# Kernel tuning notes

Hardware: AMD Instinct MI355X
Metric: run time of the kernel (lower is better)

Reference implementation:

```python
import jax, jax.numpy as jnp
import numpy as np
import math

B, D, A = 16384, 1024, 512   # batch, input_dim, n_atoms
N_ITER = 16
K_MIN = 0.01
EPS = 1e-06


def _soft(z, th):
    # sign(z) * relu(|z| - th)
    return jnp.sign(z) * jax.nn.relu(jnp.abs(z) - th)


def setup_inputs() -> dict:
    key = jax.random.key(0)
    ks = jax.random.split(key, 16)
    def lin(k, fan_in, fan_out):
        lim = 1.0 / math.sqrt(fan_in)
        kw, kb = jax.random.split(k)
        W = jax.random.uniform(kw, (fan_in, fan_out), jnp.float32, -lim, lim)
        b = jax.random.uniform(kb, (fan_out,), jnp.float32, -lim, lim)
        return W, b
    x = jax.random.normal(ks[0], (B, D), jnp.float32)
    W_proj, b_proj = lin(ks[1], D, A)
    W_rec, _ = lin(ks[2], A, A)  # bias=False
    log_threshold = jnp.full((A,), math.log(0.1), jnp.float32)
    W_pres, _ = lin(ks[3], A, 2 * A)
    b_pres = jnp.zeros((2 * A,), jnp.float32)  # presence_head_bias_init=0
    W_sign, _ = lin(ks[4], A, A)
    b_sign = jnp.zeros((A,), jnp.float32)      # sign_head_bias_init=0
    W_g1, b_g1 = lin(ks[5], D + 1 + A, A)
    W_g2, b_g2 = lin(ks[6], A, A)
    W_k, b_k = lin(ks[7], A, A)
    W_t, b_t = lin(ks[8], A, A)
    return dict(x=x, W_proj=W_proj, b_proj=b_proj, W_rec=W_rec,
                log_threshold=log_threshold, W_pres=W_pres, b_pres=b_pres,
                W_sign=W_sign, b_sign=b_sign, W_g1=W_g1, b_g1=b_g1,
                W_g2=W_g2, b_g2=b_g2, W_k=W_k, b_k=b_k, W_t=W_t, b_t=b_t)


def reference(x, W_proj, b_proj, W_rec, log_threshold, W_pres, b_pres,
              W_sign, b_sign, W_g1, b_g1, W_g2, b_g2, W_k, b_k, W_t, b_t):
    x_flat = x.reshape(x.shape[0], -1)                      # [B, D]
    input_scale = jnp.linalg.norm(x_flat, axis=1, keepdims=True)  # [B, 1]
    x_shape = x_flat / (input_scale + EPS)

    drive = x_shape @ W_proj + b_proj                       # [B, A]
    threshold = jnp.exp(log_threshold)[None, :]             # [1, A]
    h0 = _soft(drive, threshold)

    def step(h, _):
        proposal = drive + h @ W_rec
        return _soft(proposal, threshold), None
    h_delta, _ = jax.lax.scan(step, h0, None, length=N_ITER - 1)

    shape_ctx = jax.lax.stop_gradient(h_delta)              # shape_detach_to_gamma=True
    gain_scalar = jnp.log(input_scale + EPS)                # gain_feature='log_l2'
    gamma_in = jnp.concatenate([x_flat, gain_scalar, shape_ctx], axis=1)  # [B, D+1+A]
    h_gamma = jax.nn.relu(gamma_in @ W_g1 + b_g1)
    h_gamma = jax.nn.relu(h_gamma @ W_g2 + b_g2)

    k_out = jax.nn.softplus(h_gamma @ W_k + b_k) + K_MIN    # k_max=inf -> no clamp
    theta_out = jax.nn.softplus(h_gamma @ W_t + b_t) + 1e-4

    presence_logits = (h_delta @ W_pres + b_pres).reshape(x.shape[0], A, 2)[:, :, None, :]  # [B, A, 1, 2]
    sign_scores = (h_delta @ W_sign + b_sign)[:, :, None]   # [B, A, 1]

    return (k_out[:, :, None], theta_out[:, :, None], presence_logits, sign_scores,
            input_scale[:, 0], h_delta, h_gamma)
```

## Files before the change

### kernel.cpp

```cpp
#include <hip/hip_runtime.h>
#include <hip/hip_fp8.h>

typedef __attribute__((ext_vector_type(8))) short short8;
typedef __attribute__((ext_vector_type(4))) float f32x4;

#define NB 16384
#define DDIM 1024
#define AD 512

static __device__ __forceinline__ unsigned short f2bf(float f){
  unsigned int u = __float_as_uint(f);
  u += 0x7FFFu + ((u >> 16) & 1u);
  return (unsigned short)(u >> 16);
}
static __device__ __forceinline__ float bf2f(short s){
  return __uint_as_float(((unsigned int)(unsigned short)s) << 16);
}
static __device__ __forceinline__ unsigned long long pack4(float a, float b, float c, float d){
  return (unsigned long long)f2bf(a) | ((unsigned long long)f2bf(b) << 16)
       | ((unsigned long long)f2bf(c) << 32) | ((unsigned long long)f2bf(d) << 48);
}
static __device__ __forceinline__ unsigned char f2e4(float f){
  return __hip_fp8_e4m3(f).__x;
}
static __device__ __forceinline__ unsigned int pack4f8(float a, float b, float c, float d){
  return (unsigned)f2e4(a) | ((unsigned)f2e4(b) << 8) | ((unsigned)f2e4(c) << 16) | ((unsigned)f2e4(d) << 24);
}
static __device__ __forceinline__ float softplusf(float z){
  return fmaxf(z, 0.f) + log1pf(expf(-fabsf(z)));
}
static __device__ __forceinline__ float softf(float z, float th){
  return copysignf(fmaxf(fabsf(z) - th, 0.f), z);
}

static __device__ __forceinline__ void bar_lds(){
  __builtin_amdgcn_sched_barrier(0);
  asm volatile("s_waitcnt lgkmcnt(0)" ::: "memory");
  __builtin_amdgcn_s_barrier();
  __builtin_amdgcn_sched_barrier(0);
}

__global__ void pack_all(const float* __restrict__ W_proj, const float* __restrict__ W_rec,
                         const float* __restrict__ W_pres, const float* __restrict__ W_sign,
                         const float* __restrict__ W_g1,   const float* __restrict__ W_g2,
                         const float* __restrict__ W_k,    const float* __restrict__ W_t,
                         unsigned char* __restrict__ ws){
  int t = blockIdx.x * 256 + threadIdx.x;
  const float* W; size_t off; int KS, NT, ldn, isbf; float scl = 16.f;
  if      (t < 32768) {              W = W_rec;                   off = 0;       KS = 16; NT = 32; ldn = 512;  isbf = 1; }
  else if (t < 98304) { t -= 32768;  W = W_proj;                  off = 524288;  KS = 32; NT = 32; ldn = 512;  isbf = 0; }
  else if (t < 163840){ t -= 98304;  W = W_pres;                  off = 1048576; KS = 16; NT = 64; ldn = 1024; isbf = 0; }
  else if (t < 196608){ t -= 163840; W = W_sign;                  off = 1572864; KS = 16; NT = 32; ldn = 512;  isbf = 0; }
  else if (t < 262144){ t -= 196608; W = W_g1;                    off = 1835008; KS = 32; NT = 32; ldn = 512;  isbf = 0; scl = 4.f; }
  else if (t < 294912){ t -= 262144; W = W_g1 + (size_t)1025*512; off = 2359296; KS = 16; NT = 32; ldn = 512;  isbf = 0; }
  else if (t < 327680){ t -= 294912; W = W_g2;                    off = 2621440; KS = 16; NT = 32; ldn = 512;  isbf = 0; }
  else if (t < 360448){ t -= 327680; W = W_k;                     off = 2883584; KS = 16; NT = 32; ldn = 512;  isbf = 0; }
  else if (t < 393216){ t -= 360448; W = W_t;                     off = 3145728; KS = 16; NT = 32; ldn = 512;  isbf = 0; }
  else return;
  int lane = t & 63;
  int frag = t >> 6;
  int ks = frag % KS;
  int nt = frag / KS;
  int col = nt * 16 + (lane & 15);
  int k0 = ks * 32 + ((lane >> 4) << 3);
  const float* src = W + (size_t)k0 * ldn + col;
  if (isbf){
    short8 v;
#pragma unroll
    for (int j = 0; j < 8; ++j) v[j] = (short)f2bf(src[(size_t)j * ldn]);
    *(short8*)(ws + off + ((size_t)frag * 64 + lane) * 16) = v;
  } else {
    unsigned long long v = 0;
#pragma unroll
    for (int j = 0; j < 8; ++j)
      v |= (unsigned long long)f2e4(src[(size_t)j * ldn] * scl) << (8 * j);
    *(unsigned long long*)(ws + off + ((size_t)frag * 64 + lane) * 8) = v;
  }
}

__device__ __forceinline__ void gemm_bf16(const unsigned char* __restrict__ hb,
    const unsigned char* __restrict__ A, int lane, f32x4 acc[2][4]){
  const int c16 = lane & 15;
  const int g16 = (lane >> 4) << 4;
  const int swz = ((c16 & 7) << 4) ^ g16;
  const unsigned char* bp[4];
#pragma unroll
  for (int rf = 0; rf < 4; ++rf) bp[rf] = hb + (size_t)(rf * 16 + c16) * 1024;
  const unsigned char* a0 = A + lane * 16;
  const unsigned char* a1 = A + 16 * 1024 + lane * 16;
  short8 af0 = *(const short8*)a0;
  short8 af1 = *(const short8*)a1;
#pragma unroll
  for (int ks = 0; ks < 16; ++ks){
    short8 c0 = af0, c1 = af1;
    if (ks < 15){
      a0 += 1024; a1 += 1024;
      af0 = *(const short8*)a0;
      af1 = *(const short8*)a1;
    }
    int kb = ks * 64;
    short8 b[4];
#pragma unroll
    for (int rf = 0; rf < 4; ++rf) b[rf] = *(const short8*)(bp[rf] + (kb ^ swz));
    __builtin_amdgcn_s_setprio(1);
#pragma unroll
    for (int rf = 0; rf < 4; ++rf){
      acc[0][rf] = __builtin_amdgcn_mfma_f32_16x16x32_bf16(c0, b[rf], acc[0][rf], 0, 0, 0);
      acc[1][rf] = __builtin_amdgcn_mfma_f32_16x16x32_bf16(c1, b[rf], acc[1][rf], 0, 0, 0);
    }
    __builtin_amdgcn_s_setprio(0);
  }
}

template<int KSRUN, int RS>
__device__ __forceinline__ void gemm_fp8(const unsigned char* __restrict__ bb,
    const unsigned char* __restrict__ A, int kstot, int lane, f32x4 acc[2][4]){
  const int c16 = lane & 15;
  const int g8 = (lane >> 4) << 3;
  const int swz = (c16 << 3) ^ g8;
  const unsigned char* bp[4];
#pragma unroll
  for (int rf = 0; rf < 4; ++rf) bp[rf] = bb + (size_t)(rf * 16 + c16) * RS;
  const unsigned char* a0 = A + lane * 8;
  const unsigned char* a1 = A + (size_t)kstot * 512 + lane * 8;
  long f0 = *(const long*)a0;
  long f1 = *(const long*)a1;
#pragma unroll
  for (int ks = 0; ks < KSRUN; ++ks){
    long c0 = f0, c1 = f1;
    if (ks < KSRUN - 1){
      a0 += 512; a1 += 512;
      f0 = *(const long*)a0;
      f1 = *(const long*)a1;
    }
    int kb = ks * 32;
    long b[4];
#pragma unroll
    for (int rf = 0; rf < 4; ++rf) b[rf] = *(const long*)(bp[rf] + (kb ^ swz));
    __builtin_amdgcn_s_setprio(1);
#pragma unroll
    for (int rf = 0; rf < 4; ++rf){
      acc[0][rf] = __builtin_amdgcn_mfma_f32_16x16x32_fp8_fp8(c0, b[rf], acc[0][rf], 0, 0, 0);
      acc[1][rf] = __builtin_amdgcn_mfma_f32_16x16x32_fp8_fp8(c1, b[rf], acc[1][rf], 0, 0, 0);
    }
    __builtin_amdgcn_s_setprio(0);
  }
}

template<int KSRUN, int RS>
__device__ __forceinline__ void gemm_fp8_dual(const unsigned char* __restrict__ bb,
    const unsigned char* __restrict__ A0, const unsigned char* __restrict__ A1,
    int kstot, int lane, f32x4 acc0[2][4], f32x4 acc1[2][4]){
  const int c16 = lane & 15;
  const int g8 = (lane >> 4) << 3;
  const int swz = (c16 << 3) ^ g8;
  const unsigned char* bp[4];
#pragma unroll
  for (int rf = 0; rf < 4; ++rf) bp[rf] = bb + (size_t)(rf * 16 + c16) * RS;
  const unsigned char* a00 = A0 + lane * 8;
  const unsigned char* a01 = A0 + (size_t)kstot * 512 + lane * 8;
  const unsigned char* a10 = A1 + lane * 8;
  const unsigned char* a11 = A1 + (size_t)kstot * 512 + lane * 8;
  long f00 = *(const long*)a00, f01 = *(const long*)a01;
  long f10 = *(const long*)a10, f11 = *(const long*)a11;
#pragma unroll
  for (int ks = 0; ks < KSRUN; ++ks){
    long c00 = f00, c01 = f01, c10 = f10, c11 = f11;
    if (ks < KSRUN - 1){
      a00 += 512; a01 += 512; a10 += 512; a11 += 512;
      f00 = *(const long*)a00; f01 = *(const long*)a01;
      f10 = *(const long*)a10; f11 = *(const long*)a11;
    }
    int kb = ks * 32;
    long b[4];
#pragma unroll
    for (int rf = 0; rf < 4; ++rf) b[rf] = *(const long*)(bp[rf] + (kb ^ swz));
    __builtin_amdgcn_s_setprio(1);
#pragma unroll
    for (int rf = 0; rf < 4; ++rf){
      acc0[0][rf] = __builtin_amdgcn_mfma_f32_16x16x32_fp8_fp8(c00, b[rf], acc0[0][rf], 0, 0, 0);
      acc0[1][rf] = __builtin_amdgcn_mfma_f32_16x16x32_fp8_fp8(c01, b[rf], acc0[1][rf], 0, 0, 0);
      acc1[0][rf] = __builtin_amdgcn_mfma_f32_16x16x32_fp8_fp8(c10, b[rf], acc1[0][rf], 0, 0, 0);
      acc1[1][rf] = __builtin_amdgcn_mfma_f32_16x16x32_fp8_fp8(c11, b[rf], acc1[1][rf], 0, 0, 0);
    }
    __builtin_amdgcn_s_setprio(0);
  }
}

#define ZERO_ACC(A) { _Pragma("unroll") for (int c_=0;c_<2;++c_) _Pragma("unroll") for(int r_=0;r_<4;++r_){ f32x4 z_ = {0.f,0.f,0.f,0.f}; A[c_][r_]=z_; } }

static __device__ __forceinline__ void tile_write(unsigned char* tile, int row, int colb, f32x4 v){
  *(unsigned long long*)(tile + (size_t)row * 1024 + (colb ^ ((row & 7) << 4))) = pack4(v[0], v[1], v[2], v[3]);
}

static __device__ __forceinline__ void tile_store(const unsigned char* __restrict__ tile,
    float* __restrict__ dst, int ldo, int wid, int lane){
  int row = wid * 4 + (lane >> 4);
  const unsigned char* rp = tile + (size_t)row * 1024;
  float* orow = dst + (size_t)row * ldo;
  int sw = row & 7;
  int l4 = lane & 15;
#pragma unroll
  for (int cb = 0; cb < 4; ++cb){
    short8 v = *(const short8*)(rp + ((size_t)(cb * 16 + (l4 ^ sw))) * 16);
    float* op = orow + (cb * 16 + l4) * 8;
    f32x4 lo, hi;
#pragma unroll
    for (int j = 0; j < 4; ++j){ lo[j] = bf2f(v[j]); hi[j] = bf2f(v[j + 4]); }
    __builtin_nontemporal_store(lo, (f32x4*)op);
    __builtin_nontemporal_store(hi, (f32x4*)(op + 4));
  }
}

__global__ __launch_bounds__(1024, 4) void polar_main(
    const float* __restrict__ x,
    const float* __restrict__ b_proj,
    const float* __restrict__ log_th,
    const float* __restrict__ b_pres,
    const float* __restrict__ b_sign,
    const float* __restrict__ W_g1,
    const float* __restrict__ b_g1,
    const float* __restrict__ b_g2,
    const float* __restrict__ b_k,
    const float* __restrict__ b_t,
    const unsigned char* __restrict__ ws,
    float* __restrict__ out)
{
  __shared__ __align__(128) unsigned char smem[163840];
  unsigned char* hbuf = smem;
  unsigned char* xbuf = smem + 65536;
  unsigned char* aux  = smem + 131072;
  float* recip_s = (float*)aux;
  float* gain_s  = (float*)(aux + 256);

  const unsigned char* Prec  = ws;
  const unsigned char* Pproj = ws + 524288;
  const unsigned char* Ppres = ws + 1048576;
  const unsigned char* Psign = ws + 1572864;
  const unsigned char* Pg1x  = ws + 1835008;
  const unsigned char* Pg1h  = ws + 2359296;
  const unsigned char* Pg2   = ws + 2621440;
  const unsigned char* Pk    = ws + 2883584;
  const unsigned char* Pt    = ws + 3145728;

  const int tid = threadIdx.x;
  const int lane = tid & 63;
  const int wid = tid >> 6;
  const int row0 = blockIdx.x * 64;
  const int c16 = lane & 15;
  const int g2r = (lane >> 4) << 2;

  float* out_k     = out;
  float* out_th    = out + (size_t)NB * AD;
  float* out_pres  = out + (size_t)2 * NB * AD;
  float* out_sign  = out + (size_t)4 * NB * AD;
  float* out_scale = out + (size_t)5 * NB * AD;
  float* out_hd    = out_scale + NB;
  float* out_hg    = out_hd + (size_t)NB * AD;

  {
    int r = tid >> 4, sub = tid & 15;
    const float* xr = x + (size_t)(row0 + r) * DDIM + sub * 64;
    float ss = 0.f;
#pragma unroll
    for (int i = 0; i < 8; ++i){
      f32x4 v0 = __builtin_nontemporal_load((const f32x4*)(xr + i * 8));
      f32x4 v1 = __builtin_nontemporal_load((const f32x4*)(xr + i * 8 + 4));
      ss += v0[0]*v0[0] + v0[1]*v0[1] + v0[2]*v0[2] + v0[3]*v0[3]
          + v1[0]*v1[0] + v1[1]*v1[1] + v1[2]*v1[2] + v1[3]*v1[3];
      unsigned long long w = (unsigned long long)pack4f8(v0[0]*4.f, v0[1]*4.f, v0[2]*4.f, v0[3]*4.f)
                           | ((unsigned long long)pack4f8(v1[0]*4.f, v1[1]*4.f, v1[2]*4.f, v1[3]*4.f) << 32);
      int cbyte = sub * 64 + i * 8;
      *(unsigned long long*)(xbuf + (size_t)r * 1024 + (cbyte ^ ((r & 15) << 3))) = w;
    }
    ss += __shfl_xor(ss, 1);
    ss += __shfl_xor(ss, 2);
    ss += __shfl_xor(ss, 4);
    ss += __shfl_xor(ss, 8);
    if (sub == 0){
      float norm = sqrtf(ss);
      recip_s[r] = 1.f / (norm + 1e-6f);
      gain_s[r]  = logf(norm + 1e-6f);
      __builtin_nontemporal_store(norm, out_scale + row0 + r);
    }
  }
  bar_lds();

  float rn[4], gn[4];
#pragma unroll
  for (int rf = 0; rf < 4; ++rf){
    rn[rf] = recip_s[rf * 16 + c16];
    gn[rf] = gain_s[rf * 16 + c16];
  }

  f32x4 acc[2][4];

  ZERO_ACC(acc);
  gemm_fp8<32, 1024>(xbuf, Pproj + (size_t)(wid * 2) * 32 * 512, 32, lane, acc);

  f32x4 dr[2][4];
  f32x4 th4[2];
#pragma unroll
  for (int cf = 0; cf < 2; ++cf){
    int col0 = wid * 32 + cf * 16 + g2r;
    f32x4 lt = *(const f32x4*)(log_th + col0);
    f32x4 bp = *(const f32x4*)(b_proj + col0);
#pragma unroll
    for (int r = 0; r < 4; ++r) th4[cf][r] = expf(lt[r]);
#pragma unroll
    for (int rf = 0; rf < 4; ++rf)
#pragma unroll
      for (int r = 0; r < 4; ++r)
        dr[cf][rf][r] = acc[cf][rf][r] * (rn[rf] * (1.f / 64.f)) + bp[r];
  }
#pragma unroll
  for (int cf = 0; cf < 2; ++cf){
    int colb = (wid * 32 + cf * 16 + g2r) * 2;
#pragma unroll
    for (int rf = 0; rf < 4; ++rf){
      f32x4 hv;
#pragma unroll
      for (int r = 0; r < 4; ++r) hv[r] = softf(dr[cf][rf][r], th4[cf][r]);
      tile_write(hbuf, rf * 16 + c16, colb, hv);
    }
  }
  bar_lds();

  const unsigned char* Arec = Prec + (size_t)(wid * 2) * 16 * 1024;
#pragma unroll 1
  for (int it = 0; it < 15; ++it){
    ZERO_ACC(acc);
    gemm_bf16(hbuf, Arec, lane, acc);
    bar_lds();
#pragma unroll
    for (int cf = 0; cf < 2; ++cf){
      int col0 = wid * 32 + cf * 16 + g2r;
#pragma unroll
      for (int rf = 0; rf < 4; ++rf){
        int row = rf * 16 + c16;
        f32x4 hv;
#pragma unroll
        for (int r = 0; r < 4; ++r)
          hv[r] = softf(dr[cf][rf][r] + acc[cf][rf][r], th4[cf][r]);
        tile_write(hbuf, row, col0 * 2, hv);
        if (it == 14)
          *(unsigned int*)(aux + (size_t)row * 512 + (col0 ^ (c16 << 3))) =
              pack4f8(hv[0], hv[1], hv[2], hv[3]);
      }
    }
    bar_lds();
  }

  f32x4 acc2[2][4];

  tile_store(hbuf, out_hd + (size_t)row0 * AD, AD, wid, lane);

  ZERO_ACC(acc);
  ZERO_ACC(acc2);
  gemm_fp8_dual<16, 512>(aux,
      Ppres + (size_t)(wid * 2) * 16 * 512,
      Ppres + (size_t)(32 + wid * 2) * 16 * 512, 16, lane, acc, acc2);
  bar_lds();

#pragma unroll
  for (int cf = 0; cf < 2; ++cf){
    int col0 = (wid * 2 + cf) * 16 + g2r;
    f32x4 bv = *(const f32x4*)(b_pres + col0);
    int colb = (wid * 32 + cf * 16 + g2r) * 2;
#pragma unroll
    for (int rf = 0; rf < 4; ++rf){
      f32x4 o;
#pragma unroll
      for (int r = 0; r < 4; ++r) o[r] = acc[cf][rf][r] * (1.f / 16.f) + bv[r];
      tile_write(hbuf, rf * 16 + c16, colb, o);
    }
  }
  bar_lds();
  tile_store(hbuf, out_pres + (size_t)row0 * 1024, 1024, wid, lane);

  ZERO_ACC(acc);
  gemm_fp8<16, 512>(aux, Psign + (size_t)(wid * 2) * 16 * 512, 16, lane, acc);
  bar_lds();

#pragma unroll
  for (int cf = 0; cf < 2; ++cf){
    int col0 = (32 + wid * 2 + cf) * 16 + g2r;
    f32x4 bv = *(const f32x4*)(b_pres + col0);
    int colb = (wid * 32 + cf * 16 + g2r) * 2;
#pragma unroll
    for (int rf = 0; rf < 4; ++rf){
      f32x4 o;
#pragma unroll
      for (int r = 0; r < 4; ++r) o[r] = acc2[cf][rf][r] * (1.f / 16.f) + bv[r];
      tile_write(hbuf, rf * 16 + c16, colb, o);
    }
  }
  bar_lds();
  tile_store(hbuf, out_pres + (size_t)row0 * 1024 + 512, 1024, wid, lane);
  bar_lds();

#pragma unroll
  for (int cf = 0; cf < 2; ++cf){
    int col0 = wid * 32 + cf * 16 + g2r;
    f32x4 bv = *(const f32x4*)(b_sign + col0);
#pragma unroll
    for (int rf = 0; rf < 4; ++rf){
      f32x4 o;
#pragma unroll
      for (int r = 0; r < 4; ++r) o[r] = acc[cf][rf][r] * (1.f / 16.f) + bv[r];
      tile_write(hbuf, rf * 16 + c16, col0 * 2, o);
    }
  }
  bar_lds();
  tile_store(hbuf, out_sign + (size_t)row0 * AD, AD, wid, lane);

  {
    ZERO_ACC(acc);
    gemm_fp8<32, 1024>(xbuf, Pg1x + (size_t)(wid * 2) * 32 * 512, 32, lane, acc);
    gemm_fp8<16, 512>(aux, Pg1h + (size_t)(wid * 2) * 16 * 512, 16, lane, acc);

    f32x4 bv[2], wg[2];
#pragma unroll
    for (int cf = 0; cf < 2; ++cf){
      int col0 = wid * 32 + cf * 16 + g2r;
      bv[cf] = *(const f32x4*)(b_g1 + col0);
      wg[cf] = *(const f32x4*)(W_g1 + (size_t)1024 * AD + col0);
    }
    bar_lds();
#pragma unroll
    for (int cf = 0; cf < 2; ++cf){
      int col0 = wid * 32 + cf * 16 + g2r;
#pragma unroll
      for (int rf = 0; rf < 4; ++rf){
        int row = rf * 16 + c16;
        float z0 = fmaxf(acc[cf][rf][0] * (1.f/16.f) + gn[rf] * wg[cf][0] + bv[cf][0], 0.f);
        float z1 = fmaxf(acc[cf][rf][1] * (1.f/16.f) + gn[rf] * wg[cf][1] + bv[cf][1], 0.f);
        float z2 = fmaxf(acc[cf][rf][2] * (1.f/16.f) + gn[rf] * wg[cf][2] + bv[cf][2], 0.f);
        float z3 = fmaxf(acc[cf][rf][3] * (1.f/16.f) + gn[rf] * wg[cf][3] + bv[cf][3], 0.f);
        *(unsigned int*)(aux + (size_t)row * 512 + (col0 ^ (c16 << 3))) =
            pack4f8(z0, z1, z2, z3);
      }
    }
    bar_lds();
  }

  {
    ZERO_ACC(acc);
    gemm_fp8<16, 512>(aux, Pg2 + (size_t)(wid * 2) * 16 * 512, 16, lane, acc);
    f32x4 bv[2];
#pragma unroll
    for (int cf = 0; cf < 2; ++cf)
      bv[cf] = *(const f32x4*)(b_g2 + wid * 32 + cf * 16 + g2r);
    bar_lds();
#pragma unroll
    for (int cf = 0; cf < 2; ++cf){
      int col0 = wid * 32 + cf * 16 + g2r;
#pragma unroll
      for (int rf = 0; rf < 4; ++rf){
        int row = rf * 16 + c16;
        f32x4 o;
#pragma unroll
        for (int r = 0; r < 4; ++r) o[r] = fmaxf(acc[cf][rf][r] * (1.f / 16.f) + bv[cf][r], 0.f);
        *(unsigned int*)(aux + (size_t)row * 512 + (col0 ^ (c16 << 3))) =
            pack4f8(o[0], o[1], o[2], o[3]);
        tile_write(hbuf, row, col0 * 2, o);
      }
    }
    bar_lds();
    tile_store(hbuf, out_hg + (size_t)row0 * AD, AD, wid, lane);
  }

  {
    ZERO_ACC(acc);
    ZERO_ACC(acc2);
    gemm_fp8_dual<16, 512>(aux,
        Pk + (size_t)(wid * 2) * 16 * 512,
        Pt + (size_t)(wid * 2) * 16 * 512, 16, lane, acc, acc2);
    bar_lds();
#pragma unroll
    for (int cf = 0; cf < 2; ++cf){
      int col0 = wid * 32 + cf * 16 + g2r;
      f32x4 bv = *(const f32x4*)(b_k + col0);
#pragma unroll
      for (int rf = 0; rf < 4; ++rf){
        f32x4 o;
#pragma unroll
        for (int r = 0; r < 4; ++r) o[r] = softplusf(acc[cf][rf][r] * (1.f / 16.f) + bv[r]) + 0.01f;
        tile_write(hbuf, rf * 16 + c16, col0 * 2, o);
      }
    }
    bar_lds();
    tile_store(hbuf, out_k + (size_t)row0 * AD, AD, wid, lane);
    bar_lds();
#pragma unroll
    for (int cf = 0; cf < 2; ++cf){
      int col0 = wid * 32 + cf * 16 + g2r;
      f32x4 bv = *(const f32x4*)(b_t + col0);
#pragma unroll
      for (int rf = 0; rf < 4; ++rf){
        f32x4 o;
#pragma unroll
        for (int r = 0; r < 4; ++r) o[r] = softplusf(acc2[cf][rf][r] * (1.f / 16.f) + bv[r]) + 1e-4f;
        tile_write(hbuf, rf * 16 + c16, col0 * 2, o);
      }
    }
    bar_lds();
    tile_store(hbuf, out_th + (size_t)row0 * AD, AD, wid, lane);
  }
}

extern "C" void kernel_launch(void* const* d_in, const int* in_sizes, int n_in,
                              void* d_out, int out_size, void* d_ws, size_t ws_size,
                              hipStream_t stream){
  (void)in_sizes; (void)n_in; (void)out_size; (void)ws_size;
  const float* x      = (const float*)d_in[0];
  const float* W_proj = (const float*)d_in[1];
  const float* b_proj = (const float*)d_in[2];
  const float* W_rec  = (const float*)d_in[3];
  const float* log_th = (const float*)d_in[4];
  const float* W_pres = (const float*)d_in[5];
  const float* b_pres = (const float*)d_in[6];
  const float* W_sign = (const float*)d_in[7];
  const float* b_sign = (const float*)d_in[8];
  const float* W_g1   = (const float*)d_in[9];
  const float* b_g1   = (const float*)d_in[10];
  const float* W_g2   = (const float*)d_in[11];
  const float* b_g2   = (const float*)d_in[12];
  const float* W_k    = (const float*)d_in[13];
  const float* b_k    = (const float*)d_in[14];
  const float* W_t    = (const float*)d_in[15];
  const float* b_t    = (const float*)d_in[16];

  unsigned char* ws = (unsigned char*)d_ws;
  pack_all<<<1536, 256, 0, stream>>>(W_proj, W_rec, W_pres, W_sign, W_g1, W_g2, W_k, W_t, ws);
  polar_main<<<256, 1024, 0, stream>>>(
      x, b_proj, log_th, b_pres, b_sign, W_g1, b_g1, b_g2, b_k, b_t,
      ws, (float*)d_out);
}
```

Measured before the change: 513.4 us.

## Halve rows per block and widen per-wave column tiles in fused kernel

The fused kernel now handles 32 batch rows per block with 512 threads (8 waves) instead of 64 rows with 1024 threads, launching 512 blocks. Each wave now computes 64 output columns by 32 rows rather than 32 by 64, reusing each weight fragment across two row fragments and each activation fragment across four column fragments. LDS use is halved, so more blocks can be resident per CU and the grid fills all CUs. The cost is that each block streams the full packed weights for only 32 rows, doubling total weight traffic, and the A-fragment prefetch double-buffering is dropped.

```diff
diff --git a/kernel.cpp b/kernel.cpp
--- a/kernel.cpp
+++ b/kernel.cpp
@@ -78,116 +78,95 @@
   }
 }
 
+
 __device__ __forceinline__ void gemm_bf16(const unsigned char* __restrict__ hb,
-    const unsigned char* __restrict__ A, int lane, f32x4 acc[2][4]){
+    const unsigned char* __restrict__ A, int lane, f32x4 acc[4][2]){
   const int c16 = lane & 15;
   const int g16 = (lane >> 4) << 4;
   const int swz = ((c16 & 7) << 4) ^ g16;
-  const unsigned char* bp[4];
-#pragma unroll
-  for (int rf = 0; rf < 4; ++rf) bp[rf] = hb + (size_t)(rf * 16 + c16) * 1024;
-  const unsigned char* a0 = A + lane * 16;
-  const unsigned char* a1 = A + 16 * 1024 + lane * 16;
-  short8 af0 = *(const short8*)a0;
-  short8 af1 = *(const short8*)a1;
+  const unsigned char* bp0 = hb + (size_t)c16 * 1024;
+  const unsigned char* bp1 = hb + (size_t)(16 + c16) * 1024;
+  const unsigned char* ap = A + lane * 16;
 #pragma unroll
   for (int ks = 0; ks < 16; ++ks){
-    short8 c0 = af0, c1 = af1;
-    if (ks < 15){
-      a0 += 1024; a1 += 1024;
-      af0 = *(const short8*)a0;
-      af1 = *(const short8*)a1;
-    }
     int kb = ks * 64;
-    short8 b[4];
-#pragma unroll
-    for (int rf = 0; rf < 4; ++rf) b[rf] = *(const short8*)(bp[rf] + (kb ^ swz));
+    short8 b0 = *(const short8*)(bp0 + (kb ^ swz));
+    short8 b1 = *(const short8*)(bp1 + (kb ^ swz));
+    short8 a[4];
+#pragma unroll
+    for (int cf = 0; cf < 4; ++cf) a[cf] = *(const short8*)(ap + ((size_t)cf * 16 + ks) * 1024);
     __builtin_amdgcn_s_setprio(1);
 #pragma unroll
-    for (int rf = 0; rf < 4; ++rf){
-      acc[0][rf] = __builtin_amdgcn_mfma_f32_16x16x32_bf16(c0, b[rf], acc[0][rf], 0, 0, 0);
-      acc[1][rf] = __builtin_amdgcn_mfma_f32_16x16x32_bf16(c1, b[rf], acc[1][rf], 0, 0, 0);
+    for (int cf = 0; cf < 4; ++cf){
+      acc[cf][0] = __builtin_amdgcn_mfma_f32_16x16x32_bf16(a[cf], b0, acc[cf][0], 0, 0, 0);
+      acc[cf][1] = __builtin_amdgcn_mfma_f32_16x16x32_bf16(a[cf], b1, acc[cf][1], 0, 0, 0);
     }
     __builtin_amdgcn_s_setprio(0);
   }
 }
 
-template<int KSRUN, int RS>
+template<int CF, int KSRUN, int RS>
 __device__ __forceinline__ void gemm_fp8(const unsigned char* __restrict__ bb,
-    const unsigned char* __restrict__ A, int kstot, int lane, f32x4 acc[2][4]){
+    const unsigned char* __restrict__ A, int lane, f32x4 acc[][2]){
   const int c16 = lane & 15;
   const int g8 = (lane >> 4) << 3;
   const int swz = (c16 << 3) ^ g8;
-  const unsigned char* bp[4];
-#pragma unroll
-  for (int rf = 0; rf < 4; ++rf) bp[rf] = bb + (size_t)(rf * 16 + c16) * RS;
-  const unsigned char* a0 = A + lane * 8;
-  const unsigned char* a1 = A + (size_t)kstot * 512 + lane * 8;
-  long f0 = *(const long*)a0;
-  long f1 = *(const long*)a1;
+  const unsigned char* bp0 = bb + (size_t)c16 * RS;
+  const unsigned char* bp1 = bb + (size_t)(16 + c16) * RS;
+  const unsigned char* ap = A + lane * 8;
 #pragma unroll
   for (int ks = 0; ks < KSRUN; ++ks){
-    long c0 = f0, c1 = f1;
-    if (ks < KSRUN - 1){
-      a0 += 512; a1 += 512;
-      f0 = *(const long*)a0;
-      f1 = *(const long*)a1;
-    }
     int kb = ks * 32;
-    long b[4];
-#pragma unroll
-    for (int rf = 0; rf < 4; ++rf) b[rf] = *(const long*)(bp[rf] + (kb ^ swz));
+    long b0 = *(const long*)(bp0 + (kb ^ swz));
+    long b1 = *(const long*)(bp1 + (kb ^ swz));
+    long a[CF];
+#pragma unroll
+    for (int cf = 0; cf < CF; ++cf) a[cf] = *(const long*)(ap + ((size_t)cf * KSRUN + ks) * 512);
     __builtin_amdgcn_s_setprio(1);
 #pragma unroll
-    for (int rf = 0; rf < 4; ++rf){
-      acc[0][rf] = __builtin_amdgcn_mfma_f32_16x16x32_fp8_fp8(c0, b[rf], acc[0][rf], 0, 0, 0);
-      acc[1][rf] = __builtin_amdgcn_mfma_f32_16x16x32_fp8_fp8(c1, b[rf], acc[1][rf], 0, 0, 0);
+    for (int cf = 0; cf < CF; ++cf){
+      acc[cf][0] = __builtin_amdgcn_mfma_f32_16x16x32_fp8_fp8(a[cf], b0, acc[cf][0], 0, 0, 0);
+      acc[cf][1] = __builtin_amdgcn_mfma_f32_16x16x32_fp8_fp8(a[cf], b1, acc[cf][1], 0, 0, 0);
     }
     __builtin_amdgcn_s_setprio(0);
   }
 }
 
-template<int KSRUN, int RS>
+template<int CF, int KSRUN, int RS>
 __device__ __forceinline__ void gemm_fp8_dual(const unsigned char* __restrict__ bb,
     const unsigned char* __restrict__ A0, const unsigned char* __restrict__ A1,
-    int kstot, int lane, f32x4 acc0[2][4], f32x4 acc1[2][4]){
+    int lane, f32x4 acc0[][2], f32x4 acc1[][2]){
   const int c16 = lane & 15;
   const int g8 = (lane >> 4) << 3;
   const int swz = (c16 << 3) ^ g8;
-  const unsigned char* bp[4];
-#pragma unroll
-  for (int rf = 0; rf < 4; ++rf) bp[rf] = bb + (size_t)(rf * 16 + c16) * RS;
-  const unsigned char* a00 = A0 + lane * 8;
-  const unsigned char* a01 = A0 + (size_t)kstot * 512 + lane * 8;
-  const unsigned char* a10 = A1 + lane * 8;
-  const unsigned char* a11 = A1 + (size_t)kstot * 512 + lane * 8;
-  long f00 = *(const long*)a00, f01 = *(const long*)a01;
-  long f10 = *(const long*)a10, f11 = *(const long*)a11;
+  const unsigned char* bp0 = bb + (size_t)c16 * RS;
+  const unsigned char* bp1 = bb + (size_t)(16 + c16) * RS;
+  const unsigned char* ap0 = A0 + lane * 8;
+  const unsigned char* ap1 = A1 + lane * 8;
 #pragma unroll
   for (int ks = 0; ks < KSRUN; ++ks){
-    long c00 = f00, c01 = f01, c10 = f10, c11 = f11;
-    if (ks < KSRUN - 1){
-      a00 += 512; a01 += 512; a10 += 512; a11 += 512;
-      f00 = *(const long*)a00; f01 = *(const long*)a01;
-      f10 = *(const long*)a10; f11 = *(const long*)a11;
-    }
     int kb = ks * 32;
-    long b[4];
-#pragma unroll
-    for (int rf = 0; rf < 4; ++rf) b[rf] = *(const long*)(bp[rf] + (kb ^ swz));
+    long b0 = *(const long*)(bp0 + (kb ^ swz));
+    long b1 = *(const long*)(bp1 + (kb ^ swz));
+    long a[CF], c[CF];
+#pragma unroll
+    for (int cf = 0; cf < CF; ++cf){
+      a[cf] = *(const long*)(ap0 + ((size_t)cf * KSRUN + ks) * 512);
+      c[cf] = *(const long*)(ap1 + ((size_t)cf * KSRUN + ks) * 512);
+    }
     __builtin_amdgcn_s_setprio(1);
 #pragma unroll
-    for (int rf = 0; rf < 4; ++rf){
-      acc0[0][rf] = __builtin_amdgcn_mfma_f32_16x16x32_fp8_fp8(c00, b[rf], acc0[0][rf], 0, 0, 0);
-      acc0[1][rf] = __builtin_amdgcn_mfma_f32_16x16x32_fp8_fp8(c01, b[rf], acc0[1][rf], 0, 0, 0);
-      acc1[0][rf] = __builtin_amdgcn_mfma_f32_16x16x32_fp8_fp8(c10, b[rf], acc1[0][rf], 0, 0, 0);
-      acc1[1][rf] = __builtin_amdgcn_mfma_f32_16x16x32_fp8_fp8(c11, b[rf], acc1[1][rf], 0, 0, 0);
+    for (int cf = 0; cf < CF; ++cf){
+      acc0[cf][0] = __builtin_amdgcn_mfma_f32_16x16x32_fp8_fp8(a[cf], b0, acc0[cf][0], 0, 0, 0);
+      acc0[cf][1] = __builtin_amdgcn_mfma_f32_16x16x32_fp8_fp8(a[cf], b1, acc0[cf][1], 0, 0, 0);
+      acc1[cf][0] = __builtin_amdgcn_mfma_f32_16x16x32_fp8_fp8(c[cf], b0, acc1[cf][0], 0, 0, 0);
+      acc1[cf][1] = __builtin_amdgcn_mfma_f32_16x16x32_fp8_fp8(c[cf], b1, acc1[cf][1], 0, 0, 0);
     }
     __builtin_amdgcn_s_setprio(0);
   }
 }
 
-#define ZERO_ACC(A) { _Pragma("unroll") for (int c_=0;c_<2;++c_) _Pragma("unroll") for(int r_=0;r_<4;++r_){ f32x4 z_ = {0.f,0.f,0.f,0.f}; A[c_][r_]=z_; } }
+#define ZEROA(A, CF) { _Pragma("unroll") for (int c_=0;c_<CF;++c_) _Pragma("unroll") for(int r_=0;r_<2;++r_){ f32x4 z_ = {0.f,0.f,0.f,0.f}; A[c_][r_]=z_; } }
 
 static __device__ __forceinline__ void tile_write(unsigned char* tile, int row, int colb, f32x4 v){
   *(unsigned long long*)(tile + (size_t)row * 1024 + (colb ^ ((row & 7) << 4))) = pack4(v[0], v[1], v[2], v[3]);
@@ -198,21 +177,20 @@
   int row = wid * 4 + (lane >> 4);
   const unsigned char* rp = tile + (size_t)row * 1024;
   float* orow = dst + (size_t)row * ldo;
-  int sw = row & 7;
+  int sw = (row & 7) << 4;
   int l4 = lane & 15;
 #pragma unroll
-  for (int cb = 0; cb < 4; ++cb){
-    short8 v = *(const short8*)(rp + ((size_t)(cb * 16 + (l4 ^ sw))) * 16);
-    float* op = orow + (cb * 16 + l4) * 8;
-    f32x4 lo, hi;
-#pragma unroll
-    for (int j = 0; j < 4; ++j){ lo[j] = bf2f(v[j]); hi[j] = bf2f(v[j + 4]); }
-    __builtin_nontemporal_store(lo, (f32x4*)op);
-    __builtin_nontemporal_store(hi, (f32x4*)(op + 4));
-  }
-}
-
-__global__ __launch_bounds__(1024, 4) void polar_main(
+  for (int cb = 0; cb < 8; ++cb){
+    int cbyte = cb * 128 + l4 * 8;
+    unsigned long long v = *(const unsigned long long*)(rp + (cbyte ^ sw));
+    f32x4 o;
+    o[0] = bf2f((short)v); o[1] = bf2f((short)(v >> 16));
+    o[2] = bf2f((short)(v >> 32)); o[3] = bf2f((short)(v >> 48));
+    __builtin_nontemporal_store(o, (f32x4*)(orow + cb * 64 + l4 * 4));
+  }
+}
+
+__global__ __launch_bounds__(512, 4) void polar_main(
     const float* __restrict__ x,
     const float* __restrict__ b_proj,
     const float* __restrict__ log_th,
@@ -226,12 +204,12 @@
     const unsigned char* __restrict__ ws,
     float* __restrict__ out)
 {
-  __shared__ __align__(128) unsigned char smem[163840];
+  __shared__ __align__(128) unsigned char smem[81920];
   unsigned char* hbuf = smem;
-  unsigned char* xbuf = smem + 65536;
-  unsigned char* aux  = smem + 131072;
+  unsigned char* xbuf = smem + 32768;
+  unsigned char* aux  = smem + 65536;
   float* recip_s = (float*)aux;
-  float* gain_s  = (float*)(aux + 256);
+  float* gain_s  = (float*)(aux + 128);
 
   const unsigned char* Prec  = ws;
   const unsigned char* Pproj = ws + 524288;
@@ -246,7 +224,7 @@
   const int tid = threadIdx.x;
   const int lane = tid & 63;
   const int wid = tid >> 6;
-  const int row0 = blockIdx.x * 64;
+  const int row0 = blockIdx.x * 32;
   const int c16 = lane & 15;
   const int g2r = (lane >> 4) << 2;
 
@@ -286,38 +264,38 @@
   }
   bar_lds();
 
-  float rn[4], gn[4];
-#pragma unroll
-  for (int rf = 0; rf < 4; ++rf){
+  float rn[2], gn[2];
+#pragma unroll
+  for (int rf = 0; rf < 2; ++rf){
     rn[rf] = recip_s[rf * 16 + c16];
     gn[rf] = gain_s[rf * 16 + c16];
   }
 
-  f32x4 acc[2][4];
-
-  ZERO_ACC(acc);
-  gemm_fp8<32, 1024>(xbuf, Pproj + (size_t)(wid * 2) * 32 * 512, 32, lane, acc);
-
-  f32x4 dr[2][4];
-  f32x4 th4[2];
-#pragma unroll
-  for (int cf = 0; cf < 2; ++cf){
-    int col0 = wid * 32 + cf * 16 + g2r;
+  f32x4 acc[4][2];
+
+  ZEROA(acc, 4);
+  gemm_fp8<4, 32, 1024>(xbuf, Pproj + (size_t)(wid * 4) * 32 * 512, lane, acc);
+
+  f32x4 dr[4][2];
+  f32x4 th4[4];
+#pragma unroll
+  for (int cf = 0; cf < 4; ++cf){
+    int col0 = wid * 64 + cf * 16 + g2r;
     f32x4 lt = *(const f32x4*)(log_th + col0);
     f32x4 bp = *(const f32x4*)(b_proj + col0);
 #pragma unroll
     for (int r = 0; r < 4; ++r) th4[cf][r] = expf(lt[r]);
 #pragma unroll
-    for (int rf = 0; rf < 4; ++rf)
+    for (int rf = 0; rf < 2; ++rf)
 #pragma unroll
       for (int r = 0; r < 4; ++r)
         dr[cf][rf][r] = acc[cf][rf][r] * (rn[rf] * (1.f / 64.f)) + bp[r];
   }
 #pragma unroll
-  for (int cf = 0; cf < 2; ++cf){
-    int colb = (wid * 32 + cf * 16 + g2r) * 2;
-#pragma unroll
-    for (int rf = 0; rf < 4; ++rf){
+  for (int cf = 0; cf < 4; ++cf){
+    int colb = (wid * 64 + cf * 16 + g2r) * 2;
+#pragma unroll
+    for (int rf = 0; rf < 2; ++rf){
       f32x4 hv;
 #pragma unroll
       for (int r = 0; r < 4; ++r) hv[r] = softf(dr[cf][rf][r], th4[cf][r]);
@@ -326,17 +304,17 @@
   }
   bar_lds();
 
-  const unsigned char* Arec = Prec + (size_t)(wid * 2) * 16 * 1024;
+  const unsigned char* Arec = Prec + (size_t)(wid * 4) * 16 * 1024;
 #pragma unroll 1
   for (int it = 0; it < 15; ++it){
-    ZERO_ACC(acc);
+    ZEROA(acc, 4);
     gemm_bf16(hbuf, Arec, lane, acc);
     bar_lds();
 #pragma unroll
-    for (int cf = 0; cf < 2; ++cf){
-      int col0 = wid * 32 + cf * 16 + g2r;
-#pragma unroll
-      for (int rf = 0; rf < 4; ++rf){
+    for (int cf = 0; cf < 4; ++cf){
+      int col0 = wid * 64 + cf * 16 + g2r;
+#pragma unroll
+      for (int rf = 0; rf < 2; ++rf){
         int row = rf * 16 + c16;
         f32x4 hv;
 #pragma unroll
@@ -351,48 +329,46 @@
     bar_lds();
   }
 
-  f32x4 acc2[2][4];
-
   tile_store(hbuf, out_hd + (size_t)row0 * AD, AD, wid, lane);
 
-  ZERO_ACC(acc);
-  ZERO_ACC(acc2);
-  gemm_fp8_dual<16, 512>(aux,
-      Ppres + (size_t)(wid * 2) * 16 * 512,
-      Ppres + (size_t)(32 + wid * 2) * 16 * 512, 16, lane, acc, acc2);
-  bar_lds();
-
-#pragma unroll
-  for (int cf = 0; cf < 2; ++cf){
-    int col0 = (wid * 2 + cf) * 16 + g2r;
-    f32x4 bv = *(const f32x4*)(b_pres + col0);
-    int colb = (wid * 32 + cf * 16 + g2r) * 2;
-#pragma unroll
-    for (int rf = 0; rf < 4; ++rf){
-      f32x4 o;
-#pragma unroll
-      for (int r = 0; r < 4; ++r) o[r] = acc[cf][rf][r] * (1.f / 16.f) + bv[r];
-      tile_write(hbuf, rf * 16 + c16, colb, o);
+  f32x4 accP[8][2];
+  ZEROA(accP, 8);
+  gemm_fp8<8, 16, 512>(aux, Ppres + (size_t)(wid * 8) * 16 * 512, lane, accP);
+  bar_lds();
+
+  if (wid < 4){
+#pragma unroll
+    for (int cf = 0; cf < 8; ++cf){
+      int col0 = (wid * 8 + cf) * 16 + g2r;
+      f32x4 bv = *(const f32x4*)(b_pres + col0);
+#pragma unroll
+      for (int rf = 0; rf < 2; ++rf){
+        f32x4 o;
+#pragma unroll
+        for (int r = 0; r < 4; ++r) o[r] = accP[cf][rf][r] * (1.f / 16.f) + bv[r];
+        tile_write(hbuf, rf * 16 + c16, (col0 & 511) * 2, o);
+      }
     }
   }
   bar_lds();
   tile_store(hbuf, out_pres + (size_t)row0 * 1024, 1024, wid, lane);
 
-  ZERO_ACC(acc);
-  gemm_fp8<16, 512>(aux, Psign + (size_t)(wid * 2) * 16 * 512, 16, lane, acc);
-  bar_lds();
-
-#pragma unroll
-  for (int cf = 0; cf < 2; ++cf){
-    int col0 = (32 + wid * 2 + cf) * 16 + g2r;
-    f32x4 bv = *(const f32x4*)(b_pres + col0);
-    int colb = (wid * 32 + cf * 16 + g2r) * 2;
-#pragma unroll
-    for (int rf = 0; rf < 4; ++rf){
-      f32x4 o;
-#pragma unroll
-      for (int r = 0; r < 4; ++r) o[r] = acc2[cf][rf][r] * (1.f / 16.f) + bv[r];
-      tile_write(hbuf, rf * 16 + c16, colb, o);
+  ZEROA(acc, 4);
+  gemm_fp8<4, 16, 512>(aux, Psign + (size_t)(wid * 4) * 16 * 512, lane, acc);
+  bar_lds();
+
+  if (wid >= 4){
+#pragma unroll
+    for (int cf = 0; cf < 8; ++cf){
+      int col0 = (wid * 8 + cf) * 16 + g2r;
+      f32x4 bv = *(const f32x4*)(b_pres + col0);
+#pragma unroll
+      for (int rf = 0; rf < 2; ++rf){
+        f32x4 o;
+#pragma unroll
+        for (int r = 0; r < 4; ++r) o[r] = accP[cf][rf][r] * (1.f / 16.f) + bv[r];
+        tile_write(hbuf, rf * 16 + c16, (col0 & 511) * 2, o);
+      }
     }
   }
   bar_lds();
@@ -400,11 +376,11 @@
   bar_lds();
 
 #pragma unroll
-  for (int cf = 0; cf < 2; ++cf){
-    int col0 = wid * 32 + cf * 16 + g2r;
+  for (int cf = 0; cf < 4; ++cf){
+    int col0 = wid * 64 + cf * 16 + g2r;
     f32x4 bv = *(const f32x4*)(b_sign + col0);
 #pragma unroll
-    for (int rf = 0; rf < 4; ++rf){
+    for (int rf = 0; rf < 2; ++rf){
       f32x4 o;
 #pragma unroll
       for (int r = 0; r < 4; ++r) o[r] = acc[cf][rf][r] * (1.f / 16.f) + bv[r];
@@ -415,23 +391,23 @@
   tile_store(hbuf, out_sign + (size_t)row0 * AD, AD, wid, lane);
 
   {
-    ZERO_ACC(acc);
-    gemm_fp8<32, 1024>(xbuf, Pg1x + (size_t)(wid * 2) * 32 * 512, 32, lane, acc);
-    gemm_fp8<16, 512>(aux, Pg1h + (size_t)(wid * 2) * 16 * 512, 16, lane, acc);
-
-    f32x4 bv[2], wg[2];
-#pragma unroll
-    for (int cf = 0; cf < 2; ++cf){
-      int col0 = wid * 32 + cf * 16 + g2r;
+    ZEROA(acc, 4);
+    gemm_fp8<4, 32, 1024>(xbuf, Pg1x + (size_t)(wid * 4) * 32 * 512, lane, acc);
+    gemm_fp8<4, 16, 512>(aux, Pg1h + (size_t)(wid * 4) * 16 * 512, lane, acc);
+
+    f32x4 bv[4], wg[4];
+#pragma unroll
+    for (int cf = 0; cf < 4; ++cf){
+      int col0 = wid * 64 + cf * 16 + g2r;
       bv[cf] = *(const f32x4*)(b_g1 + col0);
       wg[cf] = *(const f32x4*)(W_g1 + (size_t)1024 * AD + col0);
     }
     bar_lds();
 #pragma unroll
-    for (int cf = 0; cf < 2; ++cf){
-      int col0 = wid * 32 + cf * 16 + g2r;
-#pragma unroll
-      for (int rf = 0; rf < 4; ++rf){
+    for (int cf = 0; cf < 4; ++cf){
+      int col0 = wid * 64 + cf * 16 + g2r;
+#pragma unroll
+      for (int rf = 0; rf < 2; ++rf){
         int row = rf * 16 + c16;
         float z0 = fmaxf(acc[cf][rf][0] * (1.f/16.f) + gn[rf] * wg[cf][0] + bv[cf][0], 0.f);
         float z1 = fmaxf(acc[cf][rf][1] * (1.f/16.f) + gn[rf] * wg[cf][1] + bv[cf][1], 0.f);
@@ -445,18 +421,18 @@
   }
 
   {
-    ZERO_ACC(acc);
-    gemm_fp8<16, 512>(aux, Pg2 + (size_t)(wid * 2) * 16 * 512, 16, lane, acc);
-    f32x4 bv[2];
-#pragma unroll
-    for (int cf = 0; cf < 2; ++cf)
-      bv[cf] = *(const f32x4*)(b_g2 + wid * 32 + cf * 16 + g2r);
-    bar_lds();
-#pragma unroll
-    for (int cf = 0; cf < 2; ++cf){
-      int col0 = wid * 32 + cf * 16 + g2r;
-#pragma unroll
-      for (int rf = 0; rf < 4; ++rf){
+    ZEROA(acc, 4);
+    gemm_fp8<4, 16, 512>(aux, Pg2 + (size_t)(wid * 4) * 16 * 512, lane, acc);
+    f32x4 bv[4];
+#pragma unroll
+    for (int cf = 0; cf < 4; ++cf)
+      bv[cf] = *(const f32x4*)(b_g2 + wid * 64 + cf * 16 + g2r);
+    bar_lds();
+#pragma unroll
+    for (int cf = 0; cf < 4; ++cf){
+      int col0 = wid * 64 + cf * 16 + g2r;
+#pragma unroll
+      for (int rf = 0; rf < 2; ++rf){
         int row = rf * 16 + c16;
         f32x4 o;
 #pragma unroll
@@ -471,18 +447,19 @@
   }
 
   {
-    ZERO_ACC(acc);
-    ZERO_ACC(acc2);
-    gemm_fp8_dual<16, 512>(aux,
-        Pk + (size_t)(wid * 2) * 16 * 512,
-        Pt + (size_t)(wid * 2) * 16 * 512, 16, lane, acc, acc2);
-    bar_lds();
-#pragma unroll
-    for (int cf = 0; cf < 2; ++cf){
-      int col0 = wid * 32 + cf * 16 + g2r;
+    f32x4 acc2[4][2];
+    ZEROA(acc, 4);
+    ZEROA(acc2, 4);
+    gemm_fp8_dual<4, 16, 512>(aux,
+        Pk + (size_t)(wid * 4) * 16 * 512,
+        Pt + (size_t)(wid * 4) * 16 * 512, lane, acc, acc2);
+    bar_lds();
+#pragma unroll
+    for (int cf = 0; cf < 4; ++cf){
+      int col0 = wid * 64 + cf * 16 + g2r;
       f32x4 bv = *(const f32x4*)(b_k + col0);
 #pragma unroll
-      for (int rf = 0; rf < 4; ++rf){
+      for (int rf = 0; rf < 2; ++rf){
         f32x4 o;
 #pragma unroll
         for (int r = 0; r < 4; ++r) o[r] = softplusf(acc[cf][rf][r] * (1.f / 16.f) + bv[r]) + 0.01f;
@@ -493,11 +470,11 @@
     tile_store(hbuf, out_k + (size_t)row0 * AD, AD, wid, lane);
     bar_lds();
 #pragma unroll
-    for (int cf = 0; cf < 2; ++cf){
-      int col0 = wid * 32 + cf * 16 + g2r;
+    for (int cf = 0; cf < 4; ++cf){
+      int col0 = wid * 64 + cf * 16 + g2r;
       f32x4 bv = *(const f32x4*)(b_t + col0);
 #pragma unroll
-      for (int rf = 0; rf < 4; ++rf){
+      for (int rf = 0; rf < 2; ++rf){
         f32x4 o;
 #pragma unroll
         for (int r = 0; r < 4; ++r) o[r] = softplusf(acc2[cf][rf][r] * (1.f / 16.f) + bv[r]) + 1e-4f;
@@ -533,7 +510,7 @@
 
   unsigned char* ws = (unsigned char*)d_ws;
   pack_all<<<1536, 256, 0, stream>>>(W_proj, W_rec, W_pres, W_sign, W_g1, W_g2, W_k, W_t, ws);
-  polar_main<<<256, 1024, 0, stream>>>(
+  polar_main<<<512, 512, 0, stream>>>(
       x, b_proj, log_th, b_pres, b_sign, W_g1, b_g1, b_g2, b_k, b_t,
       ws, (float*)d_out);
 }
```

New measurement: 1.046 ms. +103.8%, slower.
